# Performance work log

Measured on AMD Instinct MI355X. Metric: run time of the kernel, lower is better.

Reference implementation:

```python
import jax, jax.numpy as jnp
import numpy as np

V, E, H, B, T = 50000, 300, 512, 256, 64
D_OUT = 3
EPS = 1e-5


def setup_inputs() -> dict:
    key = jax.random.key(0)
    ks = jax.random.split(key, 16)
    s = lambda k, shape: (jax.random.normal(k, shape, jnp.float32) * 0.05)
    return {
        "premise": jax.random.randint(ks[0], (T, B), 0, V),
        "hypothesis": jax.random.randint(ks[1], (T, B), 0, V),
        "embed": s(ks[2], (V, E)),
        "W_ih": s(ks[3], (4 * H, E)),
        "W_hh": s(ks[4], (4 * H, H)),
        "b_ih": s(ks[5], (4 * H,)),
        "b_hh": s(ks[6], (4 * H,)),
        "bn0_g": jnp.ones((4 * H,), jnp.float32),
        "bn0_b": jnp.zeros((4 * H,), jnp.float32),
        "W0": s(ks[7], (4 * H, 4 * H)),
        "b0": s(ks[8], (4 * H,)),
        "bn1_g": jnp.ones((4 * H,), jnp.float32),
        "bn1_b": jnp.zeros((4 * H,), jnp.float32),
        "W1": s(ks[9], (4 * H, 4 * H)),
        "b1": s(ks[10], (4 * H,)),
        "bno_g": jnp.ones((4 * H,), jnp.float32),
        "bno_b": jnp.zeros((4 * H,), jnp.float32),
        "Wo": s(ks[11], (D_OUT, 4 * H)),
        "bo": s(ks[12], (D_OUT,)),
    }


def _lstm_final_h(xs, W_ih, W_hh, bias):
    # xs: [T, N, E]; shared-weight LSTMCell scan, returns final hidden [N, H]
    x_proj = jnp.einsum('tne,ge->tng', xs, W_ih) + bias  # hoist input GEMM out of the recurrence
    n = xs.shape[1]
    h0 = jnp.zeros((n, H), xs.dtype)

    def step(carry, xg):
        h, c = carry
        gates = xg + h @ W_hh.T
        i, f, g, o = jnp.split(gates, 4, axis=-1)  # torch LSTMCell gate order
        c = jax.nn.sigmoid(f) * c + jax.nn.sigmoid(i) * jnp.tanh(g)
        h = jax.nn.sigmoid(o) * jnp.tanh(c)
        return (h, c), None

    (h, _), _ = jax.lax.scan(step, (h0, h0), x_proj)
    return h


def _bn(x, g, b):
    # BatchNorm1d in training mode: biased batch stats
    mu = x.mean(0)
    var = x.var(0)
    return (x - mu) * jax.lax.rsqrt(var + EPS) * g + b


def reference(premise, hypothesis, embed, W_ih, W_hh, b_ih, b_hh,
              bn0_g, bn0_b, W0, b0, bn1_g, bn1_b, W1, b1,
              bno_g, bno_b, Wo, bo):
    p = embed[premise]      # [T, B, E]
    hyp = embed[hypothesis]  # [T, B, E]
    combined = jnp.concatenate([p, hyp], axis=1)  # [T, 2B, E]
    bias = b_ih + b_hh
    h_fw = _lstm_final_h(combined, W_ih, W_hh, bias)          # forward direction
    h_bw = _lstm_final_h(combined[::-1], W_ih, W_hh, bias)    # backward direction (shared cell)
    feat = jnp.concatenate([h_fw[:B], h_bw[:B], h_fw[B:], h_bw[B:]], axis=1)  # [B, 4H]
    x = jax.nn.relu(_bn(feat, bn0_g, bn0_b) @ W0.T + b0)
    x = jax.nn.relu(_bn(x, bn1_g, bn1_b) @ W1.T + b1)
    return _bn(x, bno_g, bno_b) @ Wo.T + bo  # [B, d_out]
```

## Files before the change

kernel.cpp:

```cpp
#include <hip/hip_runtime.h>
#include <hip/hip_bf16.h>


typedef __attribute__((ext_vector_type(8))) short bf16x8;
typedef __attribute__((ext_vector_type(4))) float f32x4;
typedef __attribute__((ext_vector_type(4))) unsigned int u32x4;

#define DEVI __device__ __forceinline__

template<int N> struct IC { static constexpr int v = N; };

DEVI void async16(const void* g, void* l) {
  __builtin_amdgcn_global_load_lds((const __attribute__((address_space(1))) void*)g,
                                   (__attribute__((address_space(3))) void*)l,
                                   16, 0, 0);
}
DEVI void async16_coh(const void* g, void* l) {
  __builtin_amdgcn_global_load_lds((const __attribute__((address_space(1))) void*)g,
                                   (__attribute__((address_space(3))) void*)l,
                                   16, 0, 17);
}
DEVI void store16_coh(void* addr, u32x4 v) {
  asm volatile("global_store_dwordx4 %0, %1, off sc0 sc1" ::"v"(addr), "v"(v) : "memory");
}
template<int N> DEVI void vmwait_barrier() {
  asm volatile("s_waitcnt vmcnt(%0)" ::"i"(N) : "memory");
  __builtin_amdgcn_s_barrier();
  __builtin_amdgcn_sched_barrier(0);
}
DEVI float sigmf_(float x) { return 1.f / (1.f + __expf(-x)); }
DEVI float tanhf_(float x) {
  float a = __expf(-2.f * fabsf(x));
  float t = (1.f - a) / (1.f + a);
  return copysignf(t, x);
}
DEVI __hip_bfloat16 f2b(float x) { return __float2bfloat16(x); }
DEVI float b2f(__hip_bfloat16 x) { return __bfloat162float(x); }

__global__ void cvt_f32_bf16(const float* __restrict__ src,
                             __hip_bfloat16* __restrict__ dst, int n4) {
  int i = blockIdx.x * 256 + threadIdx.x;
  int stride = gridDim.x * 256;
  for (; i < n4; i += stride) {
    float4 v = ((const float4*)src)[i];
    union { __hip_bfloat16 h[4]; uint2 u; } o;
    o.h[0] = f2b(v.x); o.h[1] = f2b(v.y); o.h[2] = f2b(v.z); o.h[3] = f2b(v.w);
    ((uint2*)dst)[i] = o.u;
  }
}

__global__ void pack_wih(const float* __restrict__ W_ih,
                         const float* __restrict__ b_ih,
                         const float* __restrict__ b_hh,
                         __hip_bfloat16* __restrict__ WihP,
                         float* __restrict__ biasL) {
  int tid = blockIdx.x * 256 + threadIdx.x;
  int stride = gridDim.x * 256;
  for (int i = tid; i < 2048 * 320; i += stride) {
    int r = i / 320, c = i - r * 320;
    WihP[i] = (c < 300) ? f2b(W_ih[r * 300 + c]) : f2b(0.f);
  }
  if (tid < 2048) biasL[tid] = b_ih[tid] + b_hh[tid];
}

__global__ void gather_kernel(const int* __restrict__ prem, const int* __restrict__ hyp,
                              const float* __restrict__ embed,
                              __hip_bfloat16* __restrict__ Ain) {
  int row = blockIdx.x * 4 + (threadIdx.x >> 6);
  int lane = threadIdx.x & 63;
  int tt = row >> 9, n = row & 511;
  int tok = (n < 256) ? prem[tt * 256 + n] : hyp[tt * 256 + (n - 256)];
  const float4* e4 = (const float4*)(embed + (size_t)tok * 300);
  uint2* d2 = (uint2*)(Ain + (size_t)row * 320);
  for (int j = lane; j < 75; j += 64) {
    float4 v = e4[j];
    union { __hip_bfloat16 h[4]; uint2 u; } o;
    o.h[0] = f2b(v.x); o.h[1] = f2b(v.y); o.h[2] = f2b(v.z); o.h[3] = f2b(v.w);
    d2[j] = o.u;
  }
  for (int j = 75 + lane; j < 80; j += 64) d2[j] = make_uint2(0u, 0u);
}

template<int BM, int EPI>
__global__ __launch_bounds__(256)
void gemm_pipe(const __hip_bfloat16* __restrict__ A,
               const __hip_bfloat16* __restrict__ Bn,
               const float* __restrict__ bias,
               void* __restrict__ Cout, int K, int ldc) {
  constexpr int BK = 64;
  constexpr int ABYT = BM * BK * 2;
  constexpr int BBYT = 128 * BK * 2;
  constexpr int APW = BM / 32;
  constexpr int IFL = APW + 4;
  constexpr int WM = BM / 2, MT = WM / 16;
  __shared__ alignas(16) char smem[2 * ABYT + 2 * BBYT];

  const int tid = threadIdx.x, lane = tid & 63, wid = tid >> 6;
  const int wrow = wid >> 1, wcol = wid & 1;
  const int m0 = blockIdx.x * BM, n0 = blockIdx.y * 128;
  const int l8 = lane & 7, ld8 = lane >> 3;
  const int swz = (l8 ^ ld8) * 8;

  const __hip_bfloat16* Abase = A + (size_t)m0 * K;
  const __hip_bfloat16* Bbase = Bn + (size_t)n0 * K;

  f32x4 acc[MT][4];
#pragma unroll
  for (int i = 0; i < MT; ++i)
#pragma unroll
    for (int j = 0; j < 4; ++j) acc[i][j] = {0.f, 0.f, 0.f, 0.f};

  auto stage = [&](int buf, int kt) {
    const __hip_bfloat16* as = Abase + kt * BK + swz;
    char* ad = smem + buf * ABYT;
#pragma unroll
    for (int s = 0; s < APW; ++s) {
      int iss = wid * APW + s;
      async16(as + (size_t)(iss * 8 + ld8) * K, ad + iss * 1024);
    }
    const __hip_bfloat16* bs = Bbase + kt * BK + swz;
    char* bd = smem + 2 * ABYT + buf * BBYT;
#pragma unroll
    for (int s = 0; s < 4; ++s) {
      int iss = wid * 4 + s;
      async16(bs + (size_t)(iss * 8 + ld8) * K, bd + iss * 1024);
    }
  };

  const int nk = K / BK;
  stage(0, 0);
  for (int kt = 0; kt < nk; ++kt) {
    if (kt + 1 < nk) {
      stage((kt + 1) & 1, kt + 1);
      vmwait_barrier<IFL>();
    } else {
      vmwait_barrier<0>();
    }
    const __hip_bfloat16* ab = (const __hip_bfloat16*)(smem + (kt & 1) * ABYT);
    const __hip_bfloat16* bb = (const __hip_bfloat16*)(smem + 2 * ABYT + (kt & 1) * BBYT);
#pragma unroll
    for (int kk = 0; kk < BK; kk += 32) {
      bf16x8 af[MT], bf[4];
#pragma unroll
      for (int i = 0; i < MT; ++i) {
        int r = wrow * WM + i * 16 + (lane & 15);
        af[i] = *(const bf16x8*)&ab[r * BK + ((kk + (lane >> 4) * 8) ^ ((r & 7) * 8))];
      }
#pragma unroll
      for (int j = 0; j < 4; ++j) {
        int r = wcol * 64 + j * 16 + (lane & 15);
        bf[j] = *(const bf16x8*)&bb[r * BK + ((kk + (lane >> 4) * 8) ^ ((r & 7) * 8))];
      }
#pragma unroll
      for (int i = 0; i < MT; ++i)
#pragma unroll
        for (int j = 0; j < 4; ++j)
          acc[i][j] = __builtin_amdgcn_mfma_f32_16x16x32_bf16(af[i], bf[j], acc[i][j], 0, 0, 0);
    }
    __builtin_amdgcn_s_barrier();
  }
  __syncthreads();

  float* Csm = (float*)smem;
#pragma unroll
  for (int i = 0; i < MT; ++i)
#pragma unroll
    for (int j = 0; j < 4; ++j)
#pragma unroll
      for (int rr = 0; rr < 4; ++rr) {
        int row = wrow * WM + i * 16 + (lane >> 4) * 4 + rr;
        int col = wcol * 64 + j * 16 + (lane & 15);
        Csm[row * 128 + (col ^ ((row & 7) << 2))] = acc[i][j][rr];
      }
  __syncthreads();
#pragma unroll
  for (int it = 0; it < BM / 16; ++it) {
    int idx = it * 256 + tid;
    int row = idx >> 4;
    int cb = (idx & 15) * 8;
    int sw = (row & 7) << 2;
    float4 v0 = *(const float4*)&Csm[row * 128 + (cb ^ sw)];
    float4 v1 = *(const float4*)&Csm[row * 128 + ((cb + 4) ^ sw)];
    float4 b0 = *(const float4*)&bias[n0 + cb];
    float4 b1 = *(const float4*)&bias[n0 + cb + 4];
    v0.x += b0.x; v0.y += b0.y; v0.z += b0.z; v0.w += b0.w;
    v1.x += b1.x; v1.y += b1.y; v1.z += b1.z; v1.w += b1.w;
    size_t base = (size_t)(m0 + row) * ldc + n0 + cb;
    if (EPI == 0) {
      union { __hip_bfloat16 h[8]; uint4 u; } o;
      o.h[0] = f2b(v0.x); o.h[1] = f2b(v0.y); o.h[2] = f2b(v0.z); o.h[3] = f2b(v0.w);
      o.h[4] = f2b(v1.x); o.h[5] = f2b(v1.y); o.h[6] = f2b(v1.z); o.h[7] = f2b(v1.w);
      *(uint4*)&((__hip_bfloat16*)Cout)[base] = o.u;
    } else {
      v0.x = fmaxf(v0.x, 0.f); v0.y = fmaxf(v0.y, 0.f);
      v0.z = fmaxf(v0.z, 0.f); v0.w = fmaxf(v0.w, 0.f);
      v1.x = fmaxf(v1.x, 0.f); v1.y = fmaxf(v1.y, 0.f);
      v1.z = fmaxf(v1.z, 0.f); v1.w = fmaxf(v1.w, 0.f);
      *(float4*)&((float*)Cout)[base] = v0;
      *(float4*)&((float*)Cout)[base + 4] = v1;
    }
  }
}

__global__ __launch_bounds__(256, 1)
void lstm_persist(const __hip_bfloat16* __restrict__ xp,
                  const __hip_bfloat16* __restrict__ Whh,
                  __hip_bfloat16* __restrict__ hA,
                  __hip_bfloat16* __restrict__ hB,
                  int* __restrict__ ctr) {
  extern __shared__ char smem[];
  const int tid = threadIdx.x, lane = tid & 63, wid = tid >> 6;
  const int bid = blockIdx.x;
  const int grp = (bid & 7) | ((bid >> 7) << 3);
  const int jt = (bid >> 3) & 15;
  const int m0 = grp * 64;
  const int l8 = lane & 7, ld8 = lane >> 3;
  const int swz = (l8 ^ ld8) * 8;

  bf16x8 w[2][16];
  for (int h = 0; h < 2; ++h) {
#pragma unroll
    for (int kt = 0; kt < 8; ++kt)
#pragma unroll
      for (int s = 0; s < 2; ++s) {
        int iss = wid * 2 + s;
        int r = h * 64 + iss * 8 + ld8;
        int g = jt * 32 + (r >> 5) * 512 + (r & 31);
        async16(Whh + (size_t)g * 512 + kt * 64 + swz,
                smem + kt * 8192 + iss * 1024);
      }
    asm volatile("s_waitcnt vmcnt(0)" ::: "memory");
    __builtin_amdgcn_s_barrier();
    __builtin_amdgcn_sched_barrier(0);
    if ((wid >> 1) == h) {
      const __hip_bfloat16* wb = (const __hip_bfloat16*)smem;
      const int lw = wid & 1;
#pragma unroll
      for (int j = 0; j < 2; ++j)
#pragma unroll
        for (int ka = 0; ka < 16; ++ka) {
          int r = lw * 32 + j * 16 + (lane & 15);
          int kt = ka >> 1, kk = (ka & 1) * 32;
          w[j][ka] = *(const bf16x8*)&wb[kt * 4096 + r * 64 +
                                         ((kk + (lane >> 4) * 8) ^ ((r & 7) * 8))];
        }
    }
    __syncthreads();
  }

  float c_[8];
#pragma unroll
  for (int e = 0; e < 8; ++e) c_[e] = 0.f;

  const int pr = tid >> 2, pj = (tid & 3) * 8;

  for (int t = 0; t < 64; ++t) {
    const __hip_bfloat16* hin = (t & 1) ? hB : hA;
    __hip_bfloat16* hout = (t & 1) ? hA : hB;

#pragma unroll
    for (int kt = 0; kt < 8; ++kt)
#pragma unroll
      for (int s = 0; s < 2; ++s) {
        int iss = wid * 2 + s;
        async16_coh(hin + (size_t)(m0 + iss * 8 + ld8) * 512 + kt * 64 + swz,
                    smem + kt * 8192 + iss * 1024);
      }
    {
      const int rowbase = (grp < 8) ? (t * 512 + m0) : ((63 - t) * 512 + (m0 - 512));
#pragma unroll
      for (int s = 0; s < 4; ++s) {
        int iss = wid * 4 + s;
        const __hip_bfloat16* src = xp + (size_t)(rowbase + iss * 4 + (lane >> 4)) * 2048 +
                                    ((lane >> 2) & 3) * 512 + jt * 32 + (lane & 3) * 8;
        async16(src, smem + 65536 + iss * 1024);
      }
    }

    f32x4 acc[4][2];
#pragma unroll
    for (int i = 0; i < 4; ++i)
#pragma unroll
      for (int j = 0; j < 2; ++j) acc[i][j] = {0.f, 0.f, 0.f, 0.f};

    auto do_kt = [&](auto K) {
      constexpr int KT = decltype(K)::v;
      vmwait_barrier<18 - 2 * KT>();
      const __hip_bfloat16* ab = (const __hip_bfloat16*)(smem + KT * 8192);
#pragma unroll
      for (int kk = 0; kk < 64; kk += 32) {
        bf16x8 af[4];
#pragma unroll
        for (int i = 0; i < 4; ++i) {
          int r = i * 16 + (lane & 15);
          af[i] = *(const bf16x8*)&ab[r * 64 + ((kk + (lane >> 4) * 8) ^ ((r & 7) * 8))];
        }
#pragma unroll
        for (int i = 0; i < 4; ++i)
#pragma unroll
          for (int j = 0; j < 2; ++j)
            acc[i][j] = __builtin_amdgcn_mfma_f32_16x16x32_bf16(
                af[i], w[j][KT * 2 + kk / 32], acc[i][j], 0, 0, 0);
      }
    };
    do_kt(IC<0>{}); do_kt(IC<1>{}); do_kt(IC<2>{}); do_kt(IC<3>{});
    do_kt(IC<4>{}); do_kt(IC<5>{}); do_kt(IC<6>{}); do_kt(IC<7>{});

    __syncthreads();
    float* gsm = (float*)smem;
#pragma unroll
    for (int i = 0; i < 4; ++i)
#pragma unroll
      for (int j = 0; j < 2; ++j)
#pragma unroll
        for (int rr = 0; rr < 4; ++rr) {
          int row = i * 16 + (lane >> 4) * 4 + rr;
          int col = wid * 32 + j * 16 + (lane & 15);
          gsm[row * 129 + col] = acc[i][j][rr];
        }
    __syncthreads();
    asm volatile("s_waitcnt vmcnt(0)" ::: "memory");

    const __hip_bfloat16* xsm = (const __hip_bfloat16*)(smem + 65536);
    bf16x8 xi = *(const bf16x8*)&xsm[(pr * 4 + 0) * 32 + pj];
    bf16x8 xf = *(const bf16x8*)&xsm[(pr * 4 + 1) * 32 + pj];
    bf16x8 xg = *(const bf16x8*)&xsm[(pr * 4 + 2) * 32 + pj];
    bf16x8 xo = *(const bf16x8*)&xsm[(pr * 4 + 3) * 32 + pj];
    union { __hip_bfloat16 h[8]; u32x4 u; } ho;
#pragma unroll
    for (int e = 0; e < 8; ++e) {
      float gi = gsm[pr * 129 + pj + e]      + b2f(((__hip_bfloat16*)&xi)[e]);
      float gf = gsm[pr * 129 + 32 + pj + e] + b2f(((__hip_bfloat16*)&xf)[e]);
      float gg = gsm[pr * 129 + 64 + pj + e] + b2f(((__hip_bfloat16*)&xg)[e]);
      float go = gsm[pr * 129 + 96 + pj + e] + b2f(((__hip_bfloat16*)&xo)[e]);
      float cn = sigmf_(gf) * c_[e] + sigmf_(gi) * tanhf_(gg);
      float hn = sigmf_(go) * tanhf_(cn);
      c_[e] = cn;
      ho.h[e] = f2b(hn);
    }
    store16_coh(&hout[(size_t)(m0 + pr) * 512 + jt * 32 + pj], ho.u);
    asm volatile("s_waitcnt vmcnt(0)" ::: "memory");
    __syncthreads();

    if (t < 63) {
      if (tid == 0) {
        atomicAdd(&ctr[grp * 64], 1);
        const int target = 16 * (t + 1);
        while (__hip_atomic_load(&ctr[grp * 64], __ATOMIC_RELAXED,
                                 __HIP_MEMORY_SCOPE_AGENT) < target)
          __builtin_amdgcn_s_sleep(1);
      }
      __syncthreads();
    }
  }
}

__global__ void feat_kernel(const __hip_bfloat16* __restrict__ hA, float* __restrict__ feat) {
  int b = blockIdx.x;
  for (int c = threadIdx.x; c < 2048; c += 256) {
    int sec = c >> 9, j = c & 511;
    int row = (sec == 0) ? b : (sec == 1) ? 512 + b : (sec == 2) ? 256 + b : 768 + b;
    feat[b * 2048 + c] = b2f(hA[(size_t)row * 512 + j]);
  }
}

__global__ void bn_stats(const float* __restrict__ x, const float* __restrict__ g,
                         const float* __restrict__ b,
                         float* __restrict__ sc, float* __restrict__ sh) {
  int c = blockIdx.x * 256 + threadIdx.x;
  float s = 0.f, s2 = 0.f;
  for (int r = 0; r < 256; ++r) {
    float v = x[r * 2048 + c];
    s += v;
    s2 += v * v;
  }
  float mu = s * (1.f / 256.f);
  float var = s2 * (1.f / 256.f) - mu * mu;
  float rs = rsqrtf(var + 1e-5f);
  float scale = g[c] * rs;
  sc[c] = scale;
  sh[c] = b[c] - mu * scale;
}

__global__ void bn_apply(const float* __restrict__ x, const float* __restrict__ sc,
                         const float* __restrict__ sh, __hip_bfloat16* __restrict__ xn) {
  int i = blockIdx.x * 256 + threadIdx.x;
  int c = i & 2047;
  xn[i] = f2b(x[i] * sc[c] + sh[c]);
}

__global__ void final_kernel(const float* __restrict__ x2, const float* __restrict__ sc,
                             const float* __restrict__ sh, const float* __restrict__ Wo,
                             const float* __restrict__ bo, float* __restrict__ out) {
  __shared__ float red[3][256];
  int b = blockIdx.x, tid = threadIdx.x;
  float a0 = 0.f, a1 = 0.f, a2 = 0.f;
  for (int c = tid; c < 2048; c += 256) {
    float v = x2[b * 2048 + c] * sc[c] + sh[c];
    a0 += v * Wo[c];
    a1 += v * Wo[2048 + c];
    a2 += v * Wo[4096 + c];
  }
  red[0][tid] = a0; red[1][tid] = a1; red[2][tid] = a2;
  __syncthreads();
  for (int s = 128; s > 0; s >>= 1) {
    if (tid < s) {
      red[0][tid] += red[0][tid + s];
      red[1][tid] += red[1][tid + s];
      red[2][tid] += red[2][tid + s];
    }
    __syncthreads();
  }
  if (tid < 3) out[b * 3 + tid] = red[tid][0] + bo[tid];
}

extern "C" void kernel_launch(void* const* d_in, const int* in_sizes, int n_in,
                              void* d_out, int out_size, void* d_ws, size_t ws_size,
                              hipStream_t stream) {
  (void)in_sizes; (void)n_in; (void)out_size; (void)ws_size;
  const int* prem = (const int*)d_in[0];
  const int* hyp = (const int*)d_in[1];
  const float* embed = (const float*)d_in[2];
  const float* W_ih = (const float*)d_in[3];
  const float* W_hh = (const float*)d_in[4];
  const float* b_ih = (const float*)d_in[5];
  const float* b_hh = (const float*)d_in[6];
  const float* bn0g = (const float*)d_in[7];
  const float* bn0b = (const float*)d_in[8];
  const float* W0 = (const float*)d_in[9];
  const float* b0 = (const float*)d_in[10];
  const float* bn1g = (const float*)d_in[11];
  const float* bn1b = (const float*)d_in[12];
  const float* W1 = (const float*)d_in[13];
  const float* b1 = (const float*)d_in[14];
  const float* bnog = (const float*)d_in[15];
  const float* bnob = (const float*)d_in[16];
  const float* Wo = (const float*)d_in[17];
  const float* bo = (const float*)d_in[18];
  float* out = (float*)d_out;

  char* w = (char*)d_ws;
  size_t off = 0;
  auto alloc = [&](size_t bytes) {
    void* p = w + off;
    off += (bytes + 255) & ~(size_t)255;
    return p;
  };
  __hip_bfloat16* WihP = (__hip_bfloat16*)alloc((size_t)2048 * 320 * 2);
  __hip_bfloat16* Whhb = (__hip_bfloat16*)alloc((size_t)2048 * 512 * 2);
  __hip_bfloat16* W0b = (__hip_bfloat16*)alloc((size_t)2048 * 2048 * 2);
  __hip_bfloat16* W1b = (__hip_bfloat16*)alloc((size_t)2048 * 2048 * 2);
  float* biasL = (float*)alloc(2048 * 4);
  int* ctr = (int*)alloc(16 * 64 * 4);
  __hip_bfloat16* xp = (__hip_bfloat16*)alloc((size_t)32768 * 2048 * 2);
  size_t ain_off = off;
  __hip_bfloat16* Ain = (__hip_bfloat16*)alloc((size_t)32768 * 320 * 2);
  size_t end_off = off;
  off = ain_off;
  __hip_bfloat16* hA = (__hip_bfloat16*)alloc((size_t)1024 * 512 * 2);
  __hip_bfloat16* hB = (__hip_bfloat16*)alloc((size_t)1024 * 512 * 2);
  float* feat = (float*)alloc((size_t)256 * 2048 * 4);
  __hip_bfloat16* xn = (__hip_bfloat16*)alloc((size_t)256 * 2048 * 2);
  float* x1 = (float*)alloc((size_t)256 * 2048 * 4);
  float* x2 = (float*)alloc((size_t)256 * 2048 * 4);
  float* sc0 = (float*)alloc(2048 * 4);
  float* sh0 = (float*)alloc(2048 * 4);
  float* sc1 = (float*)alloc(2048 * 4);
  float* sh1 = (float*)alloc(2048 * 4);
  float* sc2 = (float*)alloc(2048 * 4);
  float* sh2 = (float*)alloc(2048 * 4);
  (void)end_off;

  (void)hipMemsetAsync(ctr, 0, 16 * 64 * 4, stream);
  pack_wih<<<512, 256, 0, stream>>>(W_ih, b_ih, b_hh, WihP, biasL);
  cvt_f32_bf16<<<1024, 256, 0, stream>>>(W_hh, Whhb, 2048 * 512 / 4);
  cvt_f32_bf16<<<2048, 256, 0, stream>>>(W0, W0b, 2048 * 2048 / 4);
  cvt_f32_bf16<<<2048, 256, 0, stream>>>(W1, W1b, 2048 * 2048 / 4);
  gather_kernel<<<8192, 256, 0, stream>>>(prem, hyp, embed, Ain);
  gemm_pipe<128, 0><<<dim3(256, 16), 256, 0, stream>>>(Ain, WihP, biasL, xp, 320, 2048);
  (void)hipMemsetAsync(hA, 0, (size_t)1024 * 512 * 2, stream);
  (void)hipFuncSetAttribute(reinterpret_cast<const void*>(lstm_persist),
                            hipFuncAttributeMaxDynamicSharedMemorySize, 81920);
  lstm_persist<<<256, 256, 81920, stream>>>(xp, Whhb, hA, hB, ctr);
  feat_kernel<<<256, 256, 0, stream>>>(hA, feat);
  bn_stats<<<8, 256, 0, stream>>>(feat, bn0g, bn0b, sc0, sh0);
  bn_apply<<<2048, 256, 0, stream>>>(feat, sc0, sh0, xn);
  gemm_pipe<64, 1><<<dim3(4, 16), 256, 0, stream>>>(xn, W0b, b0, x1, 2048, 2048);
  bn_stats<<<8, 256, 0, stream>>>(x1, bn1g, bn1b, sc1, sh1);
  bn_apply<<<2048, 256, 0, stream>>>(x1, sc1, sh1, xn);
  gemm_pipe<64, 1><<<dim3(4, 16), 256, 0, stream>>>(xn, W1b, b1, x2, 2048, 2048);
  bn_stats<<<8, 256, 0, stream>>>(x2, bnog, bnob, sc2, sh2);
  final_kernel<<<256, 256, 0, stream>>>(x2, sc2, sh2, Wo, bo, out);
}
```

Baseline: 490.3 us.

## Store input projection in MFMA fragment layout and load directly to registers

The input-projection GEMM now writes its raw accumulators in MFMA fragment order, with no LDS epilogue and no bias, via a new EPI==2 path. The LSTM kernel loads these fragments straight into registers with plain global loads instead of staging them through LDS, and adds the bias itself from preloaded registers. The gate math is remapped to the fragment layout, and h is written through an LDS staging buffer for coalesced stores. The counter wait now skips the spin when the fetch-add already reaches the target. This is meant to cut LDS traffic and epilogue work in both kernels, at the cost of an extra barrier per step and a more complex indexing scheme.

```diff
diff --git a/kernel.cpp b/kernel.cpp
--- a/kernel.cpp
+++ b/kernel.cpp
@@ -22,6 +22,11 @@
 }
 DEVI void store16_coh(void* addr, u32x4 v) {
   asm volatile("global_store_dwordx4 %0, %1, off sc0 sc1" ::"v"(addr), "v"(v) : "memory");
+}
+DEVI bf16x8 load16_pin(const void* addr) {
+  bf16x8 r;
+  asm volatile("global_load_dwordx4 %0, %1, off" : "=v"(r) : "v"(addr) : "memory");
+  return r;
 }
 template<int N> DEVI void vmwait_barrier() {
   asm volatile("s_waitcnt vmcnt(%0)" ::"i"(N) : "memory");
@@ -159,8 +164,22 @@
     }
     __builtin_amdgcn_s_barrier();
   }
+
+  if (EPI == 2) {
+#pragma unroll
+    for (int i = 0; i < MT; ++i)
+#pragma unroll
+      for (int j = 0; j < 4; ++j) {
+        union { __hip_bfloat16 h[4]; uint2 u; } o;
+#pragma unroll
+        for (int rr = 0; rr < 4; ++rr) o.h[rr] = f2b(acc[i][j][rr]);
+        size_t slot = (((size_t)blockIdx.x * 16 + blockIdx.y) * 4 + wid) * 16 + i * 4 + j;
+        *(uint2*)((char*)Cout + slot * 512 + lane * 8) = o.u;
+      }
+    return;
+  }
+
   __syncthreads();
-
   float* Csm = (float*)smem;
 #pragma unroll
   for (int i = 0; i < MT; ++i)
@@ -183,28 +202,20 @@
     float4 v1 = *(const float4*)&Csm[row * 128 + ((cb + 4) ^ sw)];
     float4 b0 = *(const float4*)&bias[n0 + cb];
     float4 b1 = *(const float4*)&bias[n0 + cb + 4];
-    v0.x += b0.x; v0.y += b0.y; v0.z += b0.z; v0.w += b0.w;
-    v1.x += b1.x; v1.y += b1.y; v1.z += b1.z; v1.w += b1.w;
+    v0.x = fmaxf(v0.x + b0.x, 0.f); v0.y = fmaxf(v0.y + b0.y, 0.f);
+    v0.z = fmaxf(v0.z + b0.z, 0.f); v0.w = fmaxf(v0.w + b0.w, 0.f);
+    v1.x = fmaxf(v1.x + b1.x, 0.f); v1.y = fmaxf(v1.y + b1.y, 0.f);
+    v1.z = fmaxf(v1.z + b1.z, 0.f); v1.w = fmaxf(v1.w + b1.w, 0.f);
     size_t base = (size_t)(m0 + row) * ldc + n0 + cb;
-    if (EPI == 0) {
-      union { __hip_bfloat16 h[8]; uint4 u; } o;
-      o.h[0] = f2b(v0.x); o.h[1] = f2b(v0.y); o.h[2] = f2b(v0.z); o.h[3] = f2b(v0.w);
-      o.h[4] = f2b(v1.x); o.h[5] = f2b(v1.y); o.h[6] = f2b(v1.z); o.h[7] = f2b(v1.w);
-      *(uint4*)&((__hip_bfloat16*)Cout)[base] = o.u;
-    } else {
-      v0.x = fmaxf(v0.x, 0.f); v0.y = fmaxf(v0.y, 0.f);
-      v0.z = fmaxf(v0.z, 0.f); v0.w = fmaxf(v0.w, 0.f);
-      v1.x = fmaxf(v1.x, 0.f); v1.y = fmaxf(v1.y, 0.f);
-      v1.z = fmaxf(v1.z, 0.f); v1.w = fmaxf(v1.w, 0.f);
-      *(float4*)&((float*)Cout)[base] = v0;
-      *(float4*)&((float*)Cout)[base + 4] = v1;
-    }
+    *(float4*)&((float*)Cout)[base] = v0;
+    *(float4*)&((float*)Cout)[base + 4] = v1;
   }
 }
 
 __global__ __launch_bounds__(256, 1)
 void lstm_persist(const __hip_bfloat16* __restrict__ xp,
                   const __hip_bfloat16* __restrict__ Whh,
+                  const float* __restrict__ biasL,
                   __hip_bfloat16* __restrict__ hA,
                   __hip_bfloat16* __restrict__ hB,
                   int* __restrict__ ctr) {
@@ -248,11 +259,27 @@
     __syncthreads();
   }
 
+  const int jsel = (lane >> 5) & 1;
+  const int qx = (lane >> 3) & 3;
+  const int lane_x = (lane & 31) * 2;
+  const int lane_lo = (lane & 7) * 2;
+  const int col5b = jsel * 16 + lane_lo;
+  const int wrx = grp & 1;
+  const int wcx = (jt & 3) >> 1;
+  const int widx = wrx * 2 + wcx;
+  const int jx = (jt & 1) * 2 + jsel;
+  const int ntb = jt >> 2;
+
+  float bias_[4][2];
+#pragma unroll
+  for (int g = 0; g < 4; ++g)
+#pragma unroll
+    for (int cc = 0; cc < 2; ++cc)
+      bias_[g][cc] = biasL[g * 512 + jt * 32 + col5b + cc];
+
   float c_[8];
 #pragma unroll
   for (int e = 0; e < 8; ++e) c_[e] = 0.f;
-
-  const int pr = tid >> 2, pj = (tid & 3) * 8;
 
   for (int t = 0; t < 64; ++t) {
     const __hip_bfloat16* hin = (t & 1) ? hB : hA;
@@ -266,16 +293,16 @@
         async16_coh(hin + (size_t)(m0 + iss * 8 + ld8) * 512 + kt * 64 + swz,
                     smem + kt * 8192 + iss * 1024);
       }
-    {
-      const int rowbase = (grp < 8) ? (t * 512 + m0) : ((63 - t) * 512 + (m0 - 512));
-#pragma unroll
-      for (int s = 0; s < 4; ++s) {
-        int iss = wid * 4 + s;
-        const __hip_bfloat16* src = xp + (size_t)(rowbase + iss * 4 + (lane >> 4)) * 2048 +
-                                    ((lane >> 2) & 3) * 512 + jt * 32 + (lane & 3) * 8;
-        async16(src, smem + 65536 + iss * 1024);
-      }
-    }
+    __builtin_amdgcn_sched_barrier(0);
+    const int xrow = (grp < 8) ? (t * 512 + m0) : ((63 - t) * 512 + (m0 - 512));
+    const int mt2 = xrow >> 7;
+    bf16x8 xg_[4];
+#pragma unroll
+    for (int g = 0; g < 4; ++g) {
+      size_t slot = (((size_t)mt2 * 16 + g * 4 + ntb) * 4 + widx) * 16 + wid * 4 + jx;
+      xg_[g] = load16_pin((const char*)xp + slot * 512 + lane_x * 8);
+    }
+    __builtin_amdgcn_sched_barrier(0);
 
     f32x4 acc[4][2];
 #pragma unroll
@@ -308,6 +335,7 @@
 
     __syncthreads();
     float* gsm = (float*)smem;
+    __hip_bfloat16* hsm = (__hip_bfloat16*)(smem + 40960);
 #pragma unroll
     for (int i = 0; i < 4; ++i)
 #pragma unroll
@@ -320,35 +348,46 @@
         }
     __syncthreads();
     asm volatile("s_waitcnt vmcnt(0)" ::: "memory");
-
-    const __hip_bfloat16* xsm = (const __hip_bfloat16*)(smem + 65536);
-    bf16x8 xi = *(const bf16x8*)&xsm[(pr * 4 + 0) * 32 + pj];
-    bf16x8 xf = *(const bf16x8*)&xsm[(pr * 4 + 1) * 32 + pj];
-    bf16x8 xg = *(const bf16x8*)&xsm[(pr * 4 + 2) * 32 + pj];
-    bf16x8 xo = *(const bf16x8*)&xsm[(pr * 4 + 3) * 32 + pj];
-    union { __hip_bfloat16 h[8]; u32x4 u; } ho;
-#pragma unroll
-    for (int e = 0; e < 8; ++e) {
-      float gi = gsm[pr * 129 + pj + e]      + b2f(((__hip_bfloat16*)&xi)[e]);
-      float gf = gsm[pr * 129 + 32 + pj + e] + b2f(((__hip_bfloat16*)&xf)[e]);
-      float gg = gsm[pr * 129 + 64 + pj + e] + b2f(((__hip_bfloat16*)&xg)[e]);
-      float go = gsm[pr * 129 + 96 + pj + e] + b2f(((__hip_bfloat16*)&xo)[e]);
-      float cn = sigmf_(gf) * c_[e] + sigmf_(gi) * tanhf_(gg);
-      float hn = sigmf_(go) * tanhf_(cn);
-      c_[e] = cn;
-      ho.h[e] = f2b(hn);
-    }
-    store16_coh(&hout[(size_t)(m0 + pr) * 512 + jt * 32 + pj], ho.u);
+    __builtin_amdgcn_sched_barrier(0);
+
+    const __hip_bfloat16* x0 = (const __hip_bfloat16*)&xg_[0];
+    const __hip_bfloat16* x1 = (const __hip_bfloat16*)&xg_[1];
+    const __hip_bfloat16* x2 = (const __hip_bfloat16*)&xg_[2];
+    const __hip_bfloat16* x3 = (const __hip_bfloat16*)&xg_[3];
+#pragma unroll
+    for (int cc = 0; cc < 2; ++cc) {
+      int c5 = col5b + cc;
+#pragma unroll
+      for (int rr = 0; rr < 4; ++rr) {
+        int r = wid * 16 + qx * 4 + rr;
+        float gi = gsm[r * 129 + c5]      + b2f(x0[cc * 4 + rr]) + bias_[0][cc];
+        float gf = gsm[r * 129 + 32 + c5] + b2f(x1[cc * 4 + rr]) + bias_[1][cc];
+        float gg = gsm[r * 129 + 64 + c5] + b2f(x2[cc * 4 + rr]) + bias_[2][cc];
+        float go = gsm[r * 129 + 96 + c5] + b2f(x3[cc * 4 + rr]) + bias_[3][cc];
+        float cn = sigmf_(gf) * c_[cc * 4 + rr] + sigmf_(gi) * tanhf_(gg);
+        float hn = sigmf_(go) * tanhf_(cn);
+        c_[cc * 4 + rr] = cn;
+        hsm[r * 40 + c5] = f2b(hn);
+      }
+    }
+    __syncthreads();
+    {
+      int pr = tid >> 2, pj = (tid & 3) * 8;
+      bf16x8 hv = *(const bf16x8*)&hsm[pr * 40 + pj];
+      store16_coh(&hout[(size_t)(m0 + pr) * 512 + jt * 32 + pj], *(const u32x4*)&hv);
+    }
     asm volatile("s_waitcnt vmcnt(0)" ::: "memory");
     __syncthreads();
 
     if (t < 63) {
       if (tid == 0) {
-        atomicAdd(&ctr[grp * 64], 1);
         const int target = 16 * (t + 1);
-        while (__hip_atomic_load(&ctr[grp * 64], __ATOMIC_RELAXED,
-                                 __HIP_MEMORY_SCOPE_AGENT) < target)
-          __builtin_amdgcn_s_sleep(1);
+        int got = atomicAdd(&ctr[grp * 64], 1) + 1;
+        if (got < target) {
+          while (__hip_atomic_load(&ctr[grp * 64], __ATOMIC_RELAXED,
+                                   __HIP_MEMORY_SCOPE_AGENT) < target)
+            __builtin_amdgcn_s_sleep(1);
+        }
       }
       __syncthreads();
     }
@@ -477,11 +516,11 @@
   cvt_f32_bf16<<<2048, 256, 0, stream>>>(W0, W0b, 2048 * 2048 / 4);
   cvt_f32_bf16<<<2048, 256, 0, stream>>>(W1, W1b, 2048 * 2048 / 4);
   gather_kernel<<<8192, 256, 0, stream>>>(prem, hyp, embed, Ain);
-  gemm_pipe<128, 0><<<dim3(256, 16), 256, 0, stream>>>(Ain, WihP, biasL, xp, 320, 2048);
+  gemm_pipe<128, 2><<<dim3(256, 16), 256, 0, stream>>>(Ain, WihP, biasL, xp, 320, 2048);
   (void)hipMemsetAsync(hA, 0, (size_t)1024 * 512 * 2, stream);
   (void)hipFuncSetAttribute(reinterpret_cast<const void*>(lstm_persist),
-                            hipFuncAttributeMaxDynamicSharedMemorySize, 81920);
-  lstm_persist<<<256, 256, 81920, stream>>>(xp, Whhb, hA, hB, ctr);
+                            hipFuncAttributeMaxDynamicSharedMemorySize, 98304);
+  lstm_persist<<<256, 256, 86016, stream>>>(xp, Whhb, biasL, hA, hB, ctr);
   feat_kernel<<<256, 256, 0, stream>>>(hA, feat);
   bn_stats<<<8, 256, 0, stream>>>(feat, bn0g, bn0b, sc0, sh0);
   bn_apply<<<2048, 256, 0, stream>>>(feat, sc0, sh0, xn);
```

Measured after the change: 502.1 us. 2.4% more time.
